# Performance work log

Measured on AMD Instinct MI355X. Metric: run time of the kernel, lower is better.

## Reference

```python
import jax, jax.numpy as jnp
import numpy as np

C_IN = 34   # C*V = 2*17 channels after reshape
C_MID = 16
C_OUT = 3
N_LAYERS = 3
BN_EPS = 1e-5
NEG_SLOPE = 0.01


def setup_inputs() -> dict:
    key = jax.random.key(0)
    ks = jax.random.split(key, 16)
    B, C, T, V = 512, 2, 2048, 17
    s = 1.0 / np.sqrt(C_IN)
    inp = {
        "x": jax.random.normal(ks[0], (B, C, T, V), dtype=jnp.float32),
        # stacked per-layer 1x1-conv (linear) weights for Q/K/V of 3 attention layers
        "wq": jax.random.normal(ks[1], (N_LAYERS, C_IN, C_IN), dtype=jnp.float32) * s,
        "bq": jax.random.normal(ks[2], (N_LAYERS, C_IN), dtype=jnp.float32) * 0.02,
        "wk": jax.random.normal(ks[3], (N_LAYERS, C_IN, C_IN), dtype=jnp.float32) * s,
        "bk": jax.random.normal(ks[4], (N_LAYERS, C_IN), dtype=jnp.float32) * 0.02,
        "wv": jax.random.normal(ks[5], (N_LAYERS, C_IN, C_IN), dtype=jnp.float32) * s,
        "bv": jax.random.normal(ks[6], (N_LAYERS, C_IN), dtype=jnp.float32) * 0.02,
        # head: conv1 -> BN -> LeakyReLU -> conv2
        "w1": jax.random.normal(ks[7], (C_MID, C_IN), dtype=jnp.float32) * s,
        "b1": jax.random.normal(ks[8], (C_MID,), dtype=jnp.float32) * 0.02,
        "gamma": jnp.ones((C_MID,), dtype=jnp.float32),
        "beta": jnp.zeros((C_MID,), dtype=jnp.float32),
        "mean": jax.random.normal(ks[9], (C_MID,), dtype=jnp.float32) * 0.1,
        "var": jax.random.uniform(ks[10], (C_MID,), dtype=jnp.float32, minval=0.5, maxval=1.5),
        "w2": jax.random.normal(ks[11], (C_OUT, C_MID), dtype=jnp.float32) * (1.0 / np.sqrt(C_MID)),
        "b2": jax.random.normal(ks[12], (C_OUT,), dtype=jnp.float32) * 0.02,
    }
    return inp


def _conv1x1(w, b, h):
    # 1x1 Conv1d == linear over channel dim: (O,C) x (B,C,T) -> (B,O,T)
    return jnp.einsum('oc,bct->bot', w, h) + b[:, None]


def reference(x, wq, bq, wk, bk, wv, bv, w1, b1, gamma, beta, mean, var, w2, b2):
    B, C, T, V = x.shape
    h = x.transpose(0, 1, 3, 2).reshape(B, C * V, T)  # (B, 34, T)
    scale = 1.0 / (T ** 0.5)  # K.size(-1) ** 0.5 in the original
    for i in range(N_LAYERS):
        Q = _conv1x1(wq[i], bq[i], h)
        K = _conv1x1(wk[i], bk[i], h)
        Vv = _conv1x1(wv[i], bv[i], h)
        scores = jnp.einsum('bct,bdt->bcd', Q, K) * scale  # (B, 34, 34) channel attention
        attn = jax.nn.softmax(scores, axis=-1)
        h = jnp.einsum('bcd,bdt->bct', attn, Vv)
    y = _conv1x1(w1, b1, h)                               # (B, 16, T)
    inv = gamma / jnp.sqrt(var + BN_EPS)                  # inference-mode BatchNorm1d
    y = (y - mean[:, None]) * inv[:, None] + beta[:, None]
    y = jnp.where(y > 0, y, NEG_SLOPE * y)                # LeakyReLU
    return _conv1x1(w2, b2, y)                            # (B, 3, T)
```

## Files before the change

kernel.cpp:

```cpp
#include <hip/hip_runtime.h>

#define CV   34
#define TTOT 2048
#define NB   512
#define XB   69632
#define XC   34816

#define GS_STRIDE 1192
#define RB_OFF    (512 * 1192)
#define RB_STRIDE 1040

typedef __attribute__((ext_vector_type(8))) short v8s;
typedef __attribute__((ext_vector_type(4))) float v4f;

__device__ __forceinline__ unsigned short f2bf(float f) {
    unsigned int u = __float_as_uint(f);
    u = u + 0x7FFFu + ((u >> 16) & 1u);
    return (unsigned short)(u >> 16);
}
__device__ __forceinline__ float bf2f(unsigned short s) {
    return __uint_as_float(((unsigned int)s) << 16);
}

struct SmemGramA {
    unsigned short Hh[48][152];
    unsigned short Hl[48][152];
};
struct SmemGramB {
    float Gpart[4][34][36];
    float spart[4][36];
};

__global__ __launch_bounds__(256) void k_gram(const float* __restrict__ x,
                                              float* __restrict__ ws) {
    __shared__ union { SmemGramA a; SmemGramB b; } sm;

    const int b    = blockIdx.x >> 2;
    const int seg  = blockIdx.x & 3;
    const int tid  = threadIdx.x;
    const int l    = tid & 63;
    const int w    = tid >> 6;
    const int row16 = l & 15;
    const int quad  = l >> 4;
    const float* xb = x + (size_t)b * XB;

    v4f accG[3][3];
    v4f accS[3];
    v4f vz = {0.f, 0.f, 0.f, 0.f};
#pragma unroll
    for (int r = 0; r < 3; ++r) {
        accS[r] = vz;
#pragma unroll
        for (int c = 0; c < 3; ++c) accG[r][c] = vz;
    }
    v8s ones;
#pragma unroll
    for (int i = 0; i < 8; ++i) ones[i] = (short)0x3F80;

    for (int ch = 0; ch < 4; ++ch) {
        const int t0 = seg * 512 + ch * 128;
        __syncthreads();
        for (int i = tid; i < 1088; i += 256) {
            int co = (i >= 544);
            int j4 = i - co * 544;
            const float4 f4 = *(const float4*)(xb + co * XC + t0 * 17 + j4 * 4);
            const float fv[4] = {f4.x, f4.y, f4.z, f4.w};
#pragma unroll
            for (int e = 0; e < 4; ++e) {
                int j = j4 * 4 + e;
                int t = j / 17;
                int v = j - t * 17;
                float f = fv[e];
                unsigned short hb = f2bf(f);
                sm.a.Hh[co * 17 + v][t] = hb;
                sm.a.Hl[co * 17 + v][t] = f2bf(f - bf2f(hb));
            }
        }
        __syncthreads();
        const int koff = w * 32 + quad * 8;
        v8s fh[3], fl4[3];
#pragma unroll
        for (int r = 0; r < 3; ++r) {
            fh[r]  = *(const v8s*)&sm.a.Hh[r * 16 + row16][koff];
            fl4[r] = *(const v8s*)&sm.a.Hl[r * 16 + row16][koff];
        }
#pragma unroll
        for (int r = 0; r < 3; ++r) {
#pragma unroll
            for (int c = 0; c < 3; ++c) {
                accG[r][c] = __builtin_amdgcn_mfma_f32_16x16x32_bf16(fh[r],  fh[c],  accG[r][c], 0, 0, 0);
                accG[r][c] = __builtin_amdgcn_mfma_f32_16x16x32_bf16(fh[r],  fl4[c], accG[r][c], 0, 0, 0);
                accG[r][c] = __builtin_amdgcn_mfma_f32_16x16x32_bf16(fl4[r], fh[c],  accG[r][c], 0, 0, 0);
            }
            accS[r] = __builtin_amdgcn_mfma_f32_16x16x32_bf16(fh[r],  ones, accS[r], 0, 0, 0);
            accS[r] = __builtin_amdgcn_mfma_f32_16x16x32_bf16(fl4[r], ones, accS[r], 0, 0, 0);
        }
    }

    __syncthreads();
#pragma unroll
    for (int r = 0; r < 3; ++r) {
#pragma unroll
        for (int c = 0; c < 3; ++c) {
#pragma unroll
            for (int i = 0; i < 4; ++i) {
                int m = r * 16 + quad * 4 + i;
                int n = c * 16 + row16;
                if (m < 34 && n < 34) sm.b.Gpart[w][m][n] = accG[r][c][i];
            }
        }
        if (row16 == 0) {
#pragma unroll
            for (int i = 0; i < 4; ++i) {
                int m = r * 16 + quad * 4 + i;
                if (m < 34) sm.b.spart[w][m] = accS[r][i];
            }
        }
    }
    __syncthreads();
    float* gout = ws + (size_t)b * GS_STRIDE;
    for (int idx = tid; idx < 1156; idx += 256) {
        int m = idx / 34, n = idx - m * 34;
        atomicAdd(&gout[idx], sm.b.Gpart[0][m][n] + sm.b.Gpart[1][m][n] +
                              sm.b.Gpart[2][m][n] + sm.b.Gpart[3][m][n]);
    }
    if (tid < 34)
        atomicAdd(&gout[1156 + tid], sm.b.spart[0][tid] + sm.b.spart[1][tid] +
                                     sm.b.spart[2][tid] + sm.b.spart[3][tid]);
}


__device__ __forceinline__ void mm24(const float L[][36], const float R[][36],
                                     float D[][36], int u) {
    int ti = u / 9, tj = u - ti * 9;
    int i0 = ti * 2, j0 = tj * 4;
    float acc[2][4] = {};
    for (int e0 = 0; e0 < 36; e0 += 4) {
        float4 lv[2], rv[4];
        lv[0] = *(const float4*)&L[i0][e0];
        lv[1] = *(const float4*)&L[i0 + 1][e0];
#pragma unroll
        for (int c = 0; c < 4; ++c) rv[c] = *(const float4*)&R[j0 + c][e0];
#pragma unroll
        for (int a = 0; a < 2; ++a)
#pragma unroll
            for (int c = 0; c < 4; ++c)
                acc[a][c] += lv[a].x * rv[c].x + lv[a].y * rv[c].y +
                             lv[a].z * rv[c].z + lv[a].w * rv[c].w;
    }
#pragma unroll
    for (int a = 0; a < 2; ++a)
#pragma unroll
        for (int c = 0; c < 4; ++c) D[i0 + a][j0 + c] = acc[a][c];
}

__device__ __forceinline__ void mmG4(const float* __restrict__ Lg,
                                     const float R[][36], float D[][36],
                                     int transpose, int u) {
    int ti = u / 9, tj = u - ti * 9;
    int i0 = ti * 4, j0 = tj * 4;
    float acc[4][4] = {};
    for (int e0 = 0; e0 < 32; e0 += 4) {
        float2 la[4], lb[4];
        float4 rv[4];
#pragma unroll
        for (int a = 0; a < 4; ++a) {
            int ri = i0 + a; ri = ri < 34 ? ri : 33;
            la[a] = *(const float2*)(Lg + ri * 34 + e0);
            lb[a] = *(const float2*)(Lg + ri * 34 + e0 + 2);
        }
#pragma unroll
        for (int c = 0; c < 4; ++c) rv[c] = *(const float4*)&R[j0 + c][e0];
#pragma unroll
        for (int a = 0; a < 4; ++a)
#pragma unroll
            for (int c = 0; c < 4; ++c)
                acc[a][c] += la[a].x * rv[c].x + la[a].y * rv[c].y +
                             lb[a].x * rv[c].z + lb[a].y * rv[c].w;
    }
    {
        float2 la[4];
#pragma unroll
        for (int a = 0; a < 4; ++a) {
            int ri = i0 + a; ri = ri < 34 ? ri : 33;
            la[a] = *(const float2*)(Lg + ri * 34 + 32);
        }
#pragma unroll
        for (int c = 0; c < 4; ++c) {
            float r0 = R[j0 + c][32], r1 = R[j0 + c][33];
#pragma unroll
            for (int a = 0; a < 4; ++a) acc[a][c] += la[a].x * r0 + la[a].y * r1;
        }
    }
#pragma unroll
    for (int a = 0; a < 4; ++a) {
        if (i0 + a < 34) {
#pragma unroll
            for (int c = 0; c < 4; ++c) {
                if (transpose) D[j0 + c][i0 + a] = acc[a][c];
                else           D[i0 + a][j0 + c] = acc[a][c];
            }
        }
    }
}

__global__ __launch_bounds__(256) void k_chain(
    const float* __restrict__ wq, const float* __restrict__ bq,
    const float* __restrict__ wk, const float* __restrict__ bk,
    const float* __restrict__ wv, const float* __restrict__ bv,
    const float* __restrict__ w1, const float* __restrict__ b1,
    const float* __restrict__ gamma, const float* __restrict__ beta,
    const float* __restrict__ mean, const float* __restrict__ var,
    float* __restrict__ ws) {
    __shared__ float G0b[36][36], At[36][36], Aq[36][36], Ak[36][36],
        AvT[36][36], S1[36][36], Sc[36][36];
    __shared__ float s0v[36], a_[36], aq_[36], ak_[36], avv_[36],
        qs_[36], ks_[36], invv[16];

    const int tid = threadIdx.x;
    const int b   = blockIdx.x;
    const float* gsb = ws + (size_t)b * GS_STRIDE;

    for (int i = tid; i < 1296; i += 256) {
        int m = i / 36, n = i - m * 36;
        G0b[m][n] = 0; At[m][n] = 0; Aq[m][n] = 0; Ak[m][n] = 0;
        AvT[m][n] = 0; S1[m][n] = 0; Sc[m][n] = 0;
    }
    if (tid < 36) {
        s0v[tid] = 0; a_[tid] = 0; aq_[tid] = 0; ak_[tid] = 0; avv_[tid] = 0;
        qs_[tid] = 0; ks_[tid] = 0;
    }
    __syncthreads();
    for (int i = tid; i < 1156; i += 256) {
        int m = i / 34, n = i - m * 34;
        G0b[m][n] = gsb[i];
        Aq[m][n] = wq[i]; Ak[m][n] = wk[i]; AvT[n][m] = wv[i];
    }
    if (tid < 34) {
        s0v[tid] = gsb[1156 + tid];
        aq_[tid] = bq[tid]; ak_[tid] = bk[tid]; avv_[tid] = bv[tid];
    }
    __syncthreads();

    for (int lyr = 0; lyr < 3; ++lyr) {
        const float* wql = wq + lyr * 1156;
        const float* wkl = wk + lyr * 1156;
        const float* wvl = wv + lyr * 1156;
        if (lyr > 0) {
            if (tid < 243) {
                int g = tid / 81, u = tid - g * 81;
                const float* Lg = (g == 0) ? wql : (g == 1) ? wkl : wvl;
                float (*D)[36] = (g == 0) ? Aq : (g == 1) ? Ak : AvT;
                mmG4(Lg, At, D, g == 2, u);
            }
            __syncthreads();
        }
        if (tid < 153) {
            mm24(Aq, G0b, S1, tid);
        } else if (lyr > 0 && tid < 255) {
            int u = tid - 153, r = u / 34, c = u - r * 34;
            const float* wrow = ((r == 0) ? wql : (r == 1) ? wkl : wvl) + c * 34;
            float s = 0;
            for (int e = 0; e < 34; ++e) s += wrow[e] * a_[e];
            float bb = (r == 0) ? bq[lyr * 34 + c]
                     : (r == 1) ? bk[lyr * 34 + c] : bv[lyr * 34 + c];
            if (r == 0) aq_[c] = s + bb;
            else if (r == 1) ak_[c] = s + bb;
            else avv_[c] = s + bb;
        }
        __syncthreads();
        if (tid < 153) {
            mm24(S1, Ak, Sc, tid);
        } else if (tid >= 160 && tid < 228) {
            int u = tid - 160, r = u / 34, c = u - r * 34;
            const float (*M)[36] = r ? Ak : Aq;
            float s = 0;
            for (int e = 0; e < 34; ++e) s += M[c][e] * s0v[e];
            if (r == 0) qs_[c] = s; else ks_[c] = s;
        }
        __syncthreads();
        if (tid < 34) {
            const int c = tid;
            const float scale = 0.022097086912079608f;
            float mx = -1e30f;
            for (int d = 0; d < 34; ++d) {
                float v = (Sc[c][d] + qs_[c] * ak_[d] + aq_[c] * ks_[d] +
                           2048.0f * aq_[c] * ak_[d]) * scale;
                Sc[c][d] = v;
                mx = fmaxf(mx, v);
            }
            float sum = 0;
            for (int d = 0; d < 34; ++d) {
                float e = __expf(Sc[c][d] - mx);
                Sc[c][d] = e;
                sum += e;
            }
            float rs = 1.0f / sum;
            for (int d = 0; d < 34; ++d) Sc[c][d] *= rs;
        }
        __syncthreads();
        if (tid < 153) {
            mm24(AvT, Sc, At, tid);
        } else if (tid >= 160 && tid < 194) {
            int c = tid - 160;
            float s = 0;
            for (int d = 0; d < 34; ++d) s += Sc[c][d] * avv_[d];
            a_[c] = s;
        }
        __syncthreads();
    }

    if (tid < 72) {
        int ti = tid / 9, tj = tid - ti * 9;
        int i0 = ti * 2, j0 = tj * 4;
        float acc[2][4] = {};
        for (int e0 = 0; e0 < 32; e0 += 4) {
            float2 la[2], lb[2];
            float4 rv[4];
#pragma unroll
            for (int a = 0; a < 2; ++a) {
                la[a] = *(const float2*)(w1 + (i0 + a) * 34 + e0);
                lb[a] = *(const float2*)(w1 + (i0 + a) * 34 + e0 + 2);
            }
#pragma unroll
            for (int c = 0; c < 4; ++c) rv[c] = *(const float4*)&At[j0 + c][e0];
#pragma unroll
            for (int a = 0; a < 2; ++a)
#pragma unroll
                for (int c = 0; c < 4; ++c)
                    acc[a][c] += la[a].x * rv[c].x + la[a].y * rv[c].y +
                                 lb[a].x * rv[c].z + lb[a].y * rv[c].w;
        }
        {
            float2 la[2];
#pragma unroll
            for (int a = 0; a < 2; ++a)
                la[a] = *(const float2*)(w1 + (i0 + a) * 34 + 32);
#pragma unroll
            for (int c = 0; c < 4; ++c) {
                float r0 = At[j0 + c][32], r1 = At[j0 + c][33];
#pragma unroll
                for (int a = 0; a < 2; ++a) acc[a][c] += la[a].x * r0 + la[a].y * r1;
            }
        }
#pragma unroll
        for (int a = 0; a < 2; ++a)
#pragma unroll
            for (int c = 0; c < 4; ++c) S1[i0 + a][j0 + c] = acc[a][c];
    } else if (tid < 88) {
        int o = tid - 72;
        invv[o] = gamma[o] * rsqrtf(var[o] + 1e-5f);
    } else if (tid < 104) {
        int o = tid - 88;
        float s = 0;
        for (int e = 0; e < 34; ++e) s += w1[o * 34 + e] * a_[e];
        ks_[o] = s + b1[o];
    }
    __syncthreads();
    float* wb = ws + RB_OFF + (size_t)b * RB_STRIDE;
    if (tid < 16)
        wb[1024 + tid] = (ks_[tid] - mean[tid]) * invv[tid] + beta[tid];
    unsigned short* wp = (unsigned short*)wb;
    for (int i = tid; i < 1024; i += 256) {
        int o = i >> 6, c = i & 63;
        float vv = (c < 34) ? S1[o][c] * invv[o] : 0.0f;
        unsigned short hb = f2bf(vv);
        wp[i] = hb;
        wp[1024 + i] = f2bf(vv - bf2f(hb));
    }
}

__global__ __launch_bounds__(256) void k_out(const float* __restrict__ x,
                                             const float* __restrict__ w2,
                                             const float* __restrict__ b2,
                                             const float* __restrict__ ws,
                                             float* __restrict__ out) {
    __shared__ unsigned short HtH[128][72];
    __shared__ unsigned short HtL[128][72];

    const int tid  = threadIdx.x;
    const int b    = blockIdx.x >> 3;
    const int seg  = (blockIdx.x & 7) * 256;
    const int l    = tid & 63;
    const int w    = tid >> 6;
    const int quad = l >> 4;
    const int col  = l & 15;

    const float* wb = ws + RB_OFF + (size_t)b * RB_STRIDE;
    const unsigned short* wp = (const unsigned short*)wb;
    v8s aH[2], aL[2];
#pragma unroll
    for (int ks = 0; ks < 2; ++ks) {
        aH[ks] = *(const v8s*)&wp[col * 64 + ks * 32 + quad * 8];
        aL[ks] = *(const v8s*)&wp[1024 + col * 64 + ks * 32 + quad * 8];
    }
    float cyr[4], w2r[3][4];
#pragma unroll
    for (int i = 0; i < 4; ++i) {
        int o = quad * 4 + i;
        cyr[i] = wb[1024 + o];
#pragma unroll
        for (int p = 0; p < 3; ++p) w2r[p][i] = w2[p * 16 + o];
    }
    float b2r[3] = {b2[0], b2[1], b2[2]};
    const float* xb = x + (size_t)b * XB;

    for (int idx = tid; idx < 128 * 30; idx += 256) {
        int t = idx / 30;
        int c = 34 + (idx - t * 30);
        HtH[t][c] = 0;
        HtL[t][c] = 0;
    }

    for (int ch = 0; ch < 2; ++ch) {
        const int t0c = seg + ch * 128;
        __syncthreads();
        for (int i = tid; i < 1088; i += 256) {
            int co = (i >= 544);
            int j4 = i - co * 544;
            const float4 f4 = *(const float4*)(xb + co * XC + t0c * 17 + j4 * 4);
            const float fv[4] = {f4.x, f4.y, f4.z, f4.w};
#pragma unroll
            for (int e = 0; e < 4; ++e) {
                int j = j4 * 4 + e;
                int t = j / 17;
                int v = j - t * 17;
                float f = fv[e];
                unsigned short hb = f2bf(f);
                HtH[t][co * 17 + v] = hb;
                HtL[t][co * 17 + v] = f2bf(f - bf2f(hb));
            }
        }
        __syncthreads();
        for (int tt = w; tt < 8; tt += 4) {
            const int tBase = tt * 16;
            v4f acc = {0.f, 0.f, 0.f, 0.f};
#pragma unroll
            for (int ks = 0; ks < 2; ++ks) {
                v8s bH = *(const v8s*)&HtH[tBase + col][ks * 32 + quad * 8];
                v8s bL = *(const v8s*)&HtL[tBase + col][ks * 32 + quad * 8];
                acc = __builtin_amdgcn_mfma_f32_16x16x32_bf16(aH[ks], bH, acc, 0, 0, 0);
                acc = __builtin_amdgcn_mfma_f32_16x16x32_bf16(aH[ks], bL, acc, 0, 0, 0);
                acc = __builtin_amdgcn_mfma_f32_16x16x32_bf16(aL[ks], bH, acc, 0, 0, 0);
            }
            float op[3] = {0, 0, 0};
#pragma unroll
            for (int i = 0; i < 4; ++i) {
                float y = acc[i] + cyr[i];
                float z = (y > 0.f) ? y : 0.01f * y;
#pragma unroll
                for (int p = 0; p < 3; ++p) op[p] += w2r[p][i] * z;
            }
#pragma unroll
            for (int p = 0; p < 3; ++p) {
                op[p] += __shfl_xor(op[p], 16);
                op[p] += __shfl_xor(op[p], 32);
            }
            if (l < 16) {
                int tg = t0c + tBase + l;
#pragma unroll
                for (int p = 0; p < 3; ++p)
                    out[((size_t)b * 3 + p) * 2048 + tg] = op[p] + b2r[p];
            }
        }
    }
}

extern "C" void kernel_launch(void* const* d_in, const int* in_sizes, int n_in,
                              void* d_out, int out_size, void* d_ws, size_t ws_size,
                              hipStream_t stream) {
    const float* x     = (const float*)d_in[0];
    const float* wq    = (const float*)d_in[1];
    const float* bq    = (const float*)d_in[2];
    const float* wk    = (const float*)d_in[3];
    const float* bk    = (const float*)d_in[4];
    const float* wv    = (const float*)d_in[5];
    const float* bv    = (const float*)d_in[6];
    const float* w1    = (const float*)d_in[7];
    const float* b1    = (const float*)d_in[8];
    const float* gamma = (const float*)d_in[9];
    const float* beta  = (const float*)d_in[10];
    const float* mean  = (const float*)d_in[11];
    const float* var   = (const float*)d_in[12];
    const float* w2    = (const float*)d_in[13];
    const float* b2    = (const float*)d_in[14];
    float* ws  = (float*)d_ws;
    float* out = (float*)d_out;

    hipMemsetAsync(d_ws, 0, (size_t)NB * GS_STRIDE * sizeof(float), stream);
    k_gram<<<dim3(2048), dim3(256), 0, stream>>>(x, ws);
    k_chain<<<dim3(512), dim3(256), 0, stream>>>(wq, bq, wk, bk, wv, bv,
                                                 w1, b1, gamma, beta, mean, var, ws);
    k_out<<<dim3(4096), dim3(256), 0, stream>>>(x, w2, b2, ws, out);
}
```

Baseline: 333.8 us.

## Split Gram and output kernels into 16 time segments with partial-sum buffers

The Gram kernel now runs one block per 128-step time segment (16 per batch) and writes per-segment partial Gram matrices and row sums to workspace instead of atomically adding into a zeroed buffer. The chain kernel reduces the 16 partials itself, which removes the memset and the atomics. The output kernel is also split into 16 single-chunk blocks per batch. This raises parallelism and drops the intra-block chunk loop and atomic contention. In exchange it writes more workspace traffic, adds a 16-way reduction read in the chain kernel, and uses more blocks that each load only one tile.

```diff
diff --git a/kernel.cpp b/kernel.cpp
--- a/kernel.cpp
+++ b/kernel.cpp
@@ -6,8 +6,9 @@
 #define XB   69632
 #define XC   34816
 
-#define GS_STRIDE 1192
-#define RB_OFF    (512 * 1192)
+#define NSEG      16
+#define P_STRIDE  1200
+#define RB_OFF    (NB * NSEG * P_STRIDE)
 #define RB_STRIDE 1040
 
 typedef __attribute__((ext_vector_type(8))) short v8s;
@@ -22,21 +23,14 @@
     return __uint_as_float(((unsigned int)s) << 16);
 }
 
-struct SmemGramA {
-    unsigned short Hh[48][152];
-    unsigned short Hl[48][152];
-};
-struct SmemGramB {
-    float Gpart[4][34][36];
-    float spart[4][36];
-};
-
 __global__ __launch_bounds__(256) void k_gram(const float* __restrict__ x,
                                               float* __restrict__ ws) {
-    __shared__ union { SmemGramA a; SmemGramB b; } sm;
-
-    const int b    = blockIdx.x >> 2;
-    const int seg  = blockIdx.x & 3;
+    __shared__ unsigned short Hh[48][152];
+    __shared__ unsigned short Hl[48][152];
+
+    const int b    = blockIdx.x >> 4;
+    const int sg   = blockIdx.x & 15;
+    const int t0   = sg * 128;
     const int tid  = threadIdx.x;
     const int l    = tid & 63;
     const int w    = tid >> 6;
@@ -44,91 +38,78 @@
     const int quad  = l >> 4;
     const float* xb = x + (size_t)b * XB;
 
-    v4f accG[3][3];
-    v4f accS[3];
+    for (int i = tid; i < 1088; i += 256) {
+        int co = (i >= 544);
+        int j4 = i - co * 544;
+        const float4 f4 = *(const float4*)(xb + co * XC + t0 * 17 + j4 * 4);
+        const float fv[4] = {f4.x, f4.y, f4.z, f4.w};
+#pragma unroll
+        for (int e = 0; e < 4; ++e) {
+            int j = j4 * 4 + e;
+            int t = j / 17;
+            int v = j - t * 17;
+            float f = fv[e];
+            unsigned short hb = f2bf(f);
+            Hh[co * 17 + v][t] = hb;
+            Hl[co * 17 + v][t] = f2bf(f - bf2f(hb));
+        }
+    }
+    __syncthreads();
+
+    float* pout = ws + ((size_t)b * NSEG + sg) * P_STRIDE;
     v4f vz = {0.f, 0.f, 0.f, 0.f};
-#pragma unroll
-    for (int r = 0; r < 3; ++r) {
-        accS[r] = vz;
-#pragma unroll
-        for (int c = 0; c < 3; ++c) accG[r][c] = vz;
-    }
-    v8s ones;
-#pragma unroll
-    for (int i = 0; i < 8; ++i) ones[i] = (short)0x3F80;
-
-    for (int ch = 0; ch < 4; ++ch) {
-        const int t0 = seg * 512 + ch * 128;
-        __syncthreads();
-        for (int i = tid; i < 1088; i += 256) {
-            int co = (i >= 544);
-            int j4 = i - co * 544;
-            const float4 f4 = *(const float4*)(xb + co * XC + t0 * 17 + j4 * 4);
-            const float fv[4] = {f4.x, f4.y, f4.z, f4.w};
-#pragma unroll
-            for (int e = 0; e < 4; ++e) {
-                int j = j4 * 4 + e;
-                int t = j / 17;
-                int v = j - t * 17;
-                float f = fv[e];
-                unsigned short hb = f2bf(f);
-                sm.a.Hh[co * 17 + v][t] = hb;
-                sm.a.Hl[co * 17 + v][t] = f2bf(f - bf2f(hb));
-            }
-        }
-        __syncthreads();
-        const int koff = w * 32 + quad * 8;
-        v8s fh[3], fl4[3];
-#pragma unroll
-        for (int r = 0; r < 3; ++r) {
-            fh[r]  = *(const v8s*)&sm.a.Hh[r * 16 + row16][koff];
-            fl4[r] = *(const v8s*)&sm.a.Hl[r * 16 + row16][koff];
-        }
-#pragma unroll
-        for (int r = 0; r < 3; ++r) {
+
+    if (w < 3) {
+        const int r = w;
+        v4f accG[3] = {vz, vz, vz};
+        for (int ks = 0; ks < 4; ++ks) {
+            const int koff = ks * 32 + quad * 8;
+            v8s fhr = *(const v8s*)&Hh[r * 16 + row16][koff];
+            v8s flr = *(const v8s*)&Hl[r * 16 + row16][koff];
 #pragma unroll
             for (int c = 0; c < 3; ++c) {
-                accG[r][c] = __builtin_amdgcn_mfma_f32_16x16x32_bf16(fh[r],  fh[c],  accG[r][c], 0, 0, 0);
-                accG[r][c] = __builtin_amdgcn_mfma_f32_16x16x32_bf16(fh[r],  fl4[c], accG[r][c], 0, 0, 0);
-                accG[r][c] = __builtin_amdgcn_mfma_f32_16x16x32_bf16(fl4[r], fh[c],  accG[r][c], 0, 0, 0);
-            }
-            accS[r] = __builtin_amdgcn_mfma_f32_16x16x32_bf16(fh[r],  ones, accS[r], 0, 0, 0);
-            accS[r] = __builtin_amdgcn_mfma_f32_16x16x32_bf16(fl4[r], ones, accS[r], 0, 0, 0);
-        }
-    }
-
-    __syncthreads();
-#pragma unroll
-    for (int r = 0; r < 3; ++r) {
+                v8s fhc = *(const v8s*)&Hh[c * 16 + row16][koff];
+                v8s flc = *(const v8s*)&Hl[c * 16 + row16][koff];
+                accG[c] = __builtin_amdgcn_mfma_f32_16x16x32_bf16(fhr, fhc, accG[c], 0, 0, 0);
+                accG[c] = __builtin_amdgcn_mfma_f32_16x16x32_bf16(fhr, flc, accG[c], 0, 0, 0);
+                accG[c] = __builtin_amdgcn_mfma_f32_16x16x32_bf16(flr, fhc, accG[c], 0, 0, 0);
+            }
+        }
 #pragma unroll
         for (int c = 0; c < 3; ++c) {
 #pragma unroll
             for (int i = 0; i < 4; ++i) {
                 int m = r * 16 + quad * 4 + i;
                 int n = c * 16 + row16;
-                if (m < 34 && n < 34) sm.b.Gpart[w][m][n] = accG[r][c][i];
+                if (m < 34 && n < 34) pout[m * 34 + n] = accG[c][i];
+            }
+        }
+    } else {
+        v8s ones;
+#pragma unroll
+        for (int i = 0; i < 8; ++i) ones[i] = (short)0x3F80;
+        v4f accS[3] = {vz, vz, vz};
+        for (int ks = 0; ks < 4; ++ks) {
+            const int koff = ks * 32 + quad * 8;
+#pragma unroll
+            for (int r = 0; r < 3; ++r) {
+                v8s fh = *(const v8s*)&Hh[r * 16 + row16][koff];
+                v8s fl = *(const v8s*)&Hl[r * 16 + row16][koff];
+                accS[r] = __builtin_amdgcn_mfma_f32_16x16x32_bf16(fh, ones, accS[r], 0, 0, 0);
+                accS[r] = __builtin_amdgcn_mfma_f32_16x16x32_bf16(fl, ones, accS[r], 0, 0, 0);
             }
         }
         if (row16 == 0) {
 #pragma unroll
-            for (int i = 0; i < 4; ++i) {
-                int m = r * 16 + quad * 4 + i;
-                if (m < 34) sm.b.spart[w][m] = accS[r][i];
-            }
-        }
-    }
-    __syncthreads();
-    float* gout = ws + (size_t)b * GS_STRIDE;
-    for (int idx = tid; idx < 1156; idx += 256) {
-        int m = idx / 34, n = idx - m * 34;
-        atomicAdd(&gout[idx], sm.b.Gpart[0][m][n] + sm.b.Gpart[1][m][n] +
-                              sm.b.Gpart[2][m][n] + sm.b.Gpart[3][m][n]);
-    }
-    if (tid < 34)
-        atomicAdd(&gout[1156 + tid], sm.b.spart[0][tid] + sm.b.spart[1][tid] +
-                                     sm.b.spart[2][tid] + sm.b.spart[3][tid]);
-}
-
+            for (int r = 0; r < 3; ++r)
+#pragma unroll
+                for (int i = 0; i < 4; ++i) {
+                    int m = r * 16 + quad * 4 + i;
+                    if (m < 34) pout[1156 + m] = accS[r][i];
+                }
+        }
+    }
+}
 
 __device__ __forceinline__ void mm24(const float L[][36], const float R[][36],
                                      float D[][36], int u) {
@@ -219,7 +200,6 @@
 
     const int tid = threadIdx.x;
     const int b   = blockIdx.x;
-    const float* gsb = ws + (size_t)b * GS_STRIDE;
 
     for (int i = tid; i < 1296; i += 256) {
         int m = i / 36, n = i - m * 36;
@@ -231,13 +211,23 @@
         qs_[tid] = 0; ks_[tid] = 0;
     }
     __syncthreads();
+    const float* pb = ws + (size_t)b * NSEG * P_STRIDE;
+    for (int i = tid; i < 1190; i += 256) {
+        float s = 0;
+#pragma unroll
+        for (int sgi = 0; sgi < NSEG; ++sgi) s += pb[sgi * P_STRIDE + i];
+        if (i < 1156) {
+            int m = i / 34;
+            G0b[m][i - m * 34] = s;
+        } else {
+            s0v[i - 1156] = s;
+        }
+    }
     for (int i = tid; i < 1156; i += 256) {
         int m = i / 34, n = i - m * 34;
-        G0b[m][n] = gsb[i];
         Aq[m][n] = wq[i]; Ak[m][n] = wk[i]; AvT[n][m] = wv[i];
     }
     if (tid < 34) {
-        s0v[tid] = gsb[1156 + tid];
         aq_[tid] = bq[tid]; ak_[tid] = bk[tid]; avv_[tid] = bv[tid];
     }
     __syncthreads();
@@ -379,8 +369,8 @@
     __shared__ unsigned short HtL[128][72];
 
     const int tid  = threadIdx.x;
-    const int b    = blockIdx.x >> 3;
-    const int seg  = (blockIdx.x & 7) * 256;
+    const int b    = blockIdx.x >> 4;
+    const int t0   = (blockIdx.x & 15) * 128;
     const int l    = tid & 63;
     const int w    = tid >> 6;
     const int quad = l >> 4;
@@ -411,57 +401,53 @@
         HtH[t][c] = 0;
         HtL[t][c] = 0;
     }
-
-    for (int ch = 0; ch < 2; ++ch) {
-        const int t0c = seg + ch * 128;
-        __syncthreads();
-        for (int i = tid; i < 1088; i += 256) {
-            int co = (i >= 544);
-            int j4 = i - co * 544;
-            const float4 f4 = *(const float4*)(xb + co * XC + t0c * 17 + j4 * 4);
-            const float fv[4] = {f4.x, f4.y, f4.z, f4.w};
-#pragma unroll
-            for (int e = 0; e < 4; ++e) {
-                int j = j4 * 4 + e;
-                int t = j / 17;
-                int v = j - t * 17;
-                float f = fv[e];
-                unsigned short hb = f2bf(f);
-                HtH[t][co * 17 + v] = hb;
-                HtL[t][co * 17 + v] = f2bf(f - bf2f(hb));
-            }
-        }
-        __syncthreads();
-        for (int tt = w; tt < 8; tt += 4) {
-            const int tBase = tt * 16;
-            v4f acc = {0.f, 0.f, 0.f, 0.f};
-#pragma unroll
-            for (int ks = 0; ks < 2; ++ks) {
-                v8s bH = *(const v8s*)&HtH[tBase + col][ks * 32 + quad * 8];
-                v8s bL = *(const v8s*)&HtL[tBase + col][ks * 32 + quad * 8];
-                acc = __builtin_amdgcn_mfma_f32_16x16x32_bf16(aH[ks], bH, acc, 0, 0, 0);
-                acc = __builtin_amdgcn_mfma_f32_16x16x32_bf16(aH[ks], bL, acc, 0, 0, 0);
-                acc = __builtin_amdgcn_mfma_f32_16x16x32_bf16(aL[ks], bH, acc, 0, 0, 0);
-            }
-            float op[3] = {0, 0, 0};
-#pragma unroll
-            for (int i = 0; i < 4; ++i) {
-                float y = acc[i] + cyr[i];
-                float z = (y > 0.f) ? y : 0.01f * y;
-#pragma unroll
-                for (int p = 0; p < 3; ++p) op[p] += w2r[p][i] * z;
-            }
-#pragma unroll
-            for (int p = 0; p < 3; ++p) {
-                op[p] += __shfl_xor(op[p], 16);
-                op[p] += __shfl_xor(op[p], 32);
-            }
-            if (l < 16) {
-                int tg = t0c + tBase + l;
-#pragma unroll
-                for (int p = 0; p < 3; ++p)
-                    out[((size_t)b * 3 + p) * 2048 + tg] = op[p] + b2r[p];
-            }
+    for (int i = tid; i < 1088; i += 256) {
+        int co = (i >= 544);
+        int j4 = i - co * 544;
+        const float4 f4 = *(const float4*)(xb + co * XC + t0 * 17 + j4 * 4);
+        const float fv[4] = {f4.x, f4.y, f4.z, f4.w};
+#pragma unroll
+        for (int e = 0; e < 4; ++e) {
+            int j = j4 * 4 + e;
+            int t = j / 17;
+            int v = j - t * 17;
+            float f = fv[e];
+            unsigned short hb = f2bf(f);
+            HtH[t][co * 17 + v] = hb;
+            HtL[t][co * 17 + v] = f2bf(f - bf2f(hb));
+        }
+    }
+    __syncthreads();
+
+    for (int tt = w; tt < 8; tt += 4) {
+        const int tBase = tt * 16;
+        v4f acc = {0.f, 0.f, 0.f, 0.f};
+#pragma unroll
+        for (int ks = 0; ks < 2; ++ks) {
+            v8s bH = *(const v8s*)&HtH[tBase + col][ks * 32 + quad * 8];
+            v8s bL = *(const v8s*)&HtL[tBase + col][ks * 32 + quad * 8];
+            acc = __builtin_amdgcn_mfma_f32_16x16x32_bf16(aH[ks], bH, acc, 0, 0, 0);
+            acc = __builtin_amdgcn_mfma_f32_16x16x32_bf16(aH[ks], bL, acc, 0, 0, 0);
+            acc = __builtin_amdgcn_mfma_f32_16x16x32_bf16(aL[ks], bH, acc, 0, 0, 0);
+        }
+        float op[3] = {0, 0, 0};
+#pragma unroll
+        for (int i = 0; i < 4; ++i) {
+            float y = acc[i] + cyr[i];
+            float z = (y > 0.f) ? y : 0.01f * y;
+#pragma unroll
+            for (int p = 0; p < 3; ++p) op[p] += w2r[p][i] * z;
+        }
+#pragma unroll
+        for (int p = 0; p < 3; ++p) {
+            op[p] += __shfl_xor(op[p], 16);
+            op[p] += __shfl_xor(op[p], 32);
+        }
+        if (l < 16) {
+            int tg = t0 + tBase + l;
+#pragma unroll
+            for (int p = 0; p < 3; ++p)
+                out[((size_t)b * 3 + p) * 2048 + tg] = op[p] + b2r[p];
         }
     }
 }
@@ -487,9 +473,8 @@
     float* ws  = (float*)d_ws;
     float* out = (float*)d_out;
 
-    hipMemsetAsync(d_ws, 0, (size_t)NB * GS_STRIDE * sizeof(float), stream);
-    k_gram<<<dim3(2048), dim3(256), 0, stream>>>(x, ws);
-    k_chain<<<dim3(512), dim3(256), 0, stream>>>(wq, bq, wk, bk, wv, bv,
-                                                 w1, b1, gamma, beta, mean, var, ws);
-    k_out<<<dim3(4096), dim3(256), 0, stream>>>(x, w2, b2, ws, out);
-}
+    k_gram<<<dim3(NB * NSEG), dim3(256), 0, stream>>>(x, ws);
+    k_chain<<<dim3(NB), dim3(256), 0, stream>>>(wq, bq, wk, bk, wv, bv,
+                                                w1, b1, gamma, beta, mean, var, ws);
+    k_out<<<dim3(NB * NSEG), dim3(256), 0, stream>>>(x, w2, b2, ws, out);
+}
```

After: 340.3 us. Within noise of the previous version (+2.0%).
